# Optimization experiments

Hardware: AMD Instinct MI355X
Metric: run time of the kernel (lower is better)

## Reference

```python
import jax, jax.numpy as jnp
import numpy as np

DIM = 96
HID = 384
DEPTH = 5
HEADS = 8
INNER = 64 * DIM          # inner_dim = dim_head * dim per source (dim_head=64)
DH = INNER // HEADS       # per-head dim = 768
SCALE = 64 ** -0.5        # scale uses default dim_head=64, not actual per-head dim
EPS = 1e-5


def setup_inputs() -> dict:
    key = jax.random.key(0)
    ks = jax.random.split(key, 13)
    def p(k, shape, s=0.02):
        return jax.random.normal(k, shape, jnp.float32) * s
    return {
        "x": jax.random.normal(ks[0], (2, 512, DIM), jnp.float32),
        "gam_a": p(ks[1], (DEPTH, 3, DIM)),          # attention pre-norm gammas
        "Wq": p(ks[2], (DEPTH, 3, DIM, INNER)),
        "Wk": p(ks[3], (DEPTH, 3, DIM, INNER)),
        "Wv": p(ks[4], (DEPTH, 3, DIM, INNER)),
        "Wo": p(ks[5], (DEPTH, 3, INNER, DIM)),
        "gam_m": p(ks[6], (DEPTH, 2, DIM)),          # MLP pre-norm gammas
        "W1": p(ks[7], (DEPTH, 2, DIM, HID)),
        "b1": p(ks[8], (DEPTH, 2, HID)),
        "W2": p(ks[9], (DEPTH, 2, HID, DIM)),
        "b2": p(ks[10], (DEPTH, 2, DIM)),
        "gam_mid": p(ks[11], (DEPTH, DIM)),          # bare LayerNorm inside each block
        "gam_final": p(ks[12], (DIM,)),
    }


def _ln(x, g):
    # nn.LayerNorm(elementwise_affine=False) followed by x * (gamma + 1)
    mu = x.mean(-1, keepdims=True)
    var = ((x - mu) ** 2).mean(-1, keepdims=True)
    return (x - mu) * jax.lax.rsqrt(var + EPS) * (g + 1.0)


def _attn(x, g, wq, wk, wv, wo):
    b, n, _ = x.shape
    h = _ln(x, g)                                    # self.norm (reuse_attention=True)
    q = (h @ wq).reshape(b, n, HEADS, DH).transpose(0, 2, 1, 3) * SCALE
    k = (h @ wk).reshape(b, n, HEADS, DH).transpose(0, 2, 1, 3)
    v = (h @ wv).reshape(b, n, HEADS, DH).transpose(0, 2, 1, 3)
    sim = jnp.einsum("bhid,bhjd->bhij", q, k)        # [b,h,n,n]
    a = jax.nn.softmax(sim, axis=-1)                 # dropout=0.0 -> identity
    o = jnp.einsum("bhij,bhjd->bhid", a, v)
    return o.transpose(0, 2, 1, 3).reshape(b, n, INNER) @ wo


def _mlp(x, g, w1, b1_, w2, b2_):
    # LayerNorm -> Linear -> GELU(exact) -> Linear (dropouts eval-mode identity)
    h = jax.nn.gelu(_ln(x, g) @ w1 + b1_, approximate=False)
    return h @ w2 + b2_


def reference(x, gam_a, Wq, Wk, Wv, Wo, gam_m, W1, b1, W2, b2, gam_mid, gam_final):
    for d in range(DEPTH):
        x = _attn(x, gam_a[d, 0], Wq[d, 0], Wk[d, 0], Wv[d, 0], Wo[d, 0]) + x
        x = _mlp(x, gam_m[d, 0], W1[d, 0], b1[d, 0], W2[d, 0], b2[d, 0]) + x
        x = _attn(x, gam_a[d, 1], Wq[d, 1], Wk[d, 1], Wv[d, 1], Wo[d, 1]) + x
        x = _attn(x, gam_a[d, 2], Wq[d, 2], Wk[d, 2], Wv[d, 2], Wo[d, 2]) + x
        x = _ln(x, gam_mid[d])                       # bare LayerNorm, NO residual
        x = _mlp(x, gam_m[d, 1], W1[d, 1], b1[d, 1], W2[d, 1], b2[d, 1]) + x
    return _ln(x, gam_final)
```

## Files before the change

### kernel.cpp

```cpp
#include <hip/hip_runtime.h>
#include <hip/hip_bf16.h>

typedef __hip_bfloat16 bf16;
typedef __attribute__((ext_vector_type(8))) short bf16x8;
typedef __attribute__((ext_vector_type(4))) float f32x4;

#define TOK    1024
#define DIM    96
#define HIDN   384
#define HEADS  8
#define DH     768
#define INNER  6144
#define SEQ    512
#define NDEPTH 5
#define EPSLN  1e-5f
#define QSCALE 0.125f

#define MFMA16(a, b, c) __builtin_amdgcn_mfma_f32_16x16x32_bf16((a), (b), (c), 0, 0, 0)

__device__ __forceinline__ float b2f(bf16 v) { return __bfloat162float(v); }
__device__ __forceinline__ bf16  f2b(float v) { return __float2bfloat16(v); }

__device__ __forceinline__ float gload(const void* p, size_t i, int f) {
  return f ? b2f(((const bf16*)p)[i]) : ((const float*)p)[i];
}
__device__ __forceinline__ const char* gptr(const void* base, size_t off, int f) {
  return (const char*)base + off * (size_t)(f ? 2 : 4);
}

__global__ __launch_bounds__(256) void detect_kernel(const void* xraw, int* flag) {
  __shared__ int cnt[256];
  int t = threadIdx.x;
  const unsigned short* u = (const unsigned short*)xraw;
  int c = 0;
  #pragma unroll
  for (int i = 0; i < 4; i++) {
    unsigned short h = u[2 * (t * 4 + i)];
    int e = (h >> 7) & 0xFF;
    if (e >= 87 && e <= 132) c++;
  }
  cnt[t] = c;
  __syncthreads();
  for (int s = 128; s > 0; s >>= 1) {
    if (t < s) cnt[t] += cnt[t + s];
    __syncthreads();
  }
  if (t == 0) *flag = (cnt[0] > 700) ? 1 : 0;
}

__global__ __launch_bounds__(256) void castw3_kernel(
    const void* __restrict__ w0, const void* __restrict__ w1,
    const void* __restrict__ w2, bf16* __restrict__ o0,
    bf16* __restrict__ o1, bf16* __restrict__ o2, int n,
    const int* __restrict__ flagp) {
  if (*flagp) return;
  const float* in = (const float*)((blockIdx.y == 0) ? w0 : (blockIdx.y == 1) ? w1 : w2);
  bf16* out = (blockIdx.y == 0) ? o0 : (blockIdx.y == 1) ? o1 : o2;
  int i0 = (blockIdx.x * blockDim.x + threadIdx.x) * 4;
  if (i0 + 3 < n) {
    float4 v = *(const float4*)(in + i0);
    alignas(8) unsigned short o[4];
    bf16 t0 = f2b(v.x); o[0] = *(unsigned short*)&t0;
    bf16 t1 = f2b(v.y); o[1] = *(unsigned short*)&t1;
    bf16 t2 = f2b(v.z); o[2] = *(unsigned short*)&t2;
    bf16 t3 = f2b(v.w); o[3] = *(unsigned short*)&t3;
    *(uint2*)&out[i0] = *(const uint2*)o;
  } else {
    for (int i = i0; i < n; i++) out[i] = f2b(in[i]);
  }
}

__global__ __launch_bounds__(256) void wtrans_kernel(
    const void* __restrict__ src, int R, int C,
    bf16* __restrict__ dst, const int* __restrict__ flagp) {
  __shared__ float tile[32][65];
  int f = *flagp;
  int t = threadIdx.x;
  int c0 = blockIdx.x * 64, r0 = blockIdx.y * 32;
  size_t bb = (size_t)blockIdx.z * R * C;
  int ty = t >> 4, tx = t & 15;
  #pragma unroll
  for (int half = 0; half < 2; half++) {
    int r = r0 + ty + half * 16;
    int c = c0 + tx * 4;
    if (c < C) {
      size_t idx = bb + (size_t)r * C + c;
      float v0, v1, v2, v3;
      if (f) {
        uint2 u = *(const uint2*)((const unsigned short*)src + idx);
        v0 = __uint_as_float((u.x & 0xffffu) << 16);
        v1 = __uint_as_float(u.x & 0xffff0000u);
        v2 = __uint_as_float((u.y & 0xffffu) << 16);
        v3 = __uint_as_float(u.y & 0xffff0000u);
      } else {
        float4 v = *(const float4*)((const float*)src + idx);
        v0 = v.x; v1 = v.y; v2 = v.z; v3 = v.w;
      }
      tile[ty + half * 16][tx * 4 + 0] = v0;
      tile[ty + half * 16][tx * 4 + 1] = v1;
      tile[ty + half * 16][tx * 4 + 2] = v2;
      tile[ty + half * 16][tx * 4 + 3] = v3;
    }
  }
  __syncthreads();
  int cc = c0 + (t >> 2), rseg = (t & 3) * 8;
  if (cc < C) {
    int cs = cc - c0;
    alignas(16) unsigned short o[8];
    #pragma unroll
    for (int j = 0; j < 8; j++) {
      bf16 tv = f2b(tile[rseg + j][cs]);
      o[j] = *(unsigned short*)&tv;
    }
    *(uint4*)&dst[bb + (size_t)cc * R + r0 + rseg] = *(const uint4*)o;
  }
}

template <int WM>
__device__ __forceinline__ void gemm_bt_body(
    const bf16* __restrict__ A, int lda,
    const bf16* __restrict__ Bt, int ldb,
    int m0, int n0, int kbeg, int kend, int Mtot, int N,
    float alpha, bf16* __restrict__ Cb, int ldc) {
  constexpr int TM = WM * 32;
  __shared__ bf16 As[TM][40];
  __shared__ bf16 Bs[128][40];
  int t = threadIdx.x;
  int lane = t & 63;
  int wave = t >> 6;
  int wm = (wave >> 1) * (WM * 16), wn = (wave & 1) * 64;
  f32x4 acc[WM][4];
  #pragma unroll
  for (int i = 0; i < WM; i++)
    #pragma unroll
    for (int j = 0; j < 4; j++) acc[i][j] = (f32x4){0.f, 0.f, 0.f, 0.f};

  int arow = t >> 2, aseg = (t & 3) * 8;

  for (int kb = kbeg; kb < kend; kb += 32) {
    if constexpr (TM >= 64) {
      #pragma unroll
      for (int i = 0; i < TM / 64; i++) {
        int gm = min(m0 + arow + i * 64, Mtot - 1);
        *(uint4*)&As[arow + i * 64][aseg] =
            *(const uint4*)(A + (size_t)gm * lda + kb + aseg);
      }
    } else {
      if (arow < TM) {
        int gm = min(m0 + arow, Mtot - 1);
        *(uint4*)&As[arow][aseg] =
            *(const uint4*)(A + (size_t)gm * lda + kb + aseg);
      }
    }
    #pragma unroll
    for (int i = 0; i < 2; i++) {
      int r = arow + i * 64;
      int gn = n0 + r;
      uint4 val = {0, 0, 0, 0};
      if (gn < N) val = *(const uint4*)(Bt + (size_t)gn * ldb + kb + aseg);
      *(uint4*)&Bs[r][aseg] = val;
    }
    __syncthreads();
    int fm = lane & 15, fq = (lane >> 4) * 8;
    bf16x8 af[WM], bfv[4];
    #pragma unroll
    for (int i = 0; i < WM; i++)
      af[i] = *(const bf16x8*)&As[wm + i * 16 + fm][fq];
    #pragma unroll
    for (int j = 0; j < 4; j++)
      bfv[j] = *(const bf16x8*)&Bs[wn + j * 16 + fm][fq];
    #pragma unroll
    for (int i = 0; i < WM; i++)
      #pragma unroll
      for (int j = 0; j < 4; j++)
        acc[i][j] = MFMA16(af[i], bfv[j], acc[i][j]);
    __syncthreads();
  }
  int col = lane & 15, rq = (lane >> 4) * 4;
  #pragma unroll
  for (int j = 0; j < 4; j++) {
    int gn = n0 + wn + j * 16 + col;
    if (gn >= N) continue;
    #pragma unroll
    for (int i = 0; i < WM; i++) {
      #pragma unroll
      for (int r = 0; r < 4; r++) {
        int gm = m0 + wm + i * 16 + rq + r;
        if (gm >= Mtot) continue;
        Cb[(size_t)gm * ldc + gn] = f2b(acc[i][j][r] * alpha);
      }
    }
  }
}

__global__ __launch_bounds__(256) void mtgt_kernel(
    const void* __restrict__ WqE, const void* __restrict__ WkE,
    const void* __restrict__ WvE,
    const bf16* __restrict__ wqB, const bf16* __restrict__ wkB,
    const bf16* __restrict__ wvB, const bf16* __restrict__ woT,
    bf16* __restrict__ Mt, bf16* __restrict__ Gt,
    const int* __restrict__ flagp) {
  int f = *flagp;
  const bf16* wq = f ? (const bf16*)WqE : wqB;
  const bf16* wk = f ? (const bf16*)WkE : wkB;
  const bf16* wv = f ? (const bf16*)WvE : wvB;
  int z = blockIdx.z;
  bool isM = z < 120;
  int zz = isM ? z : z - 120;
  int L = zz >> 3, h = zz & 7;
  size_t wo = (size_t)L * DIM * INNER + (size_t)h * DH;
  const bf16* A  = isM ? (wk + wo) : (woT + wo);
  const bf16* Bt = isM ? (wq + wo) : (wv + wo);
  bf16* C = (isM ? Mt : Gt) + (size_t)zz * DIM * DIM;
  gemm_bt_body<2>(A, INNER, Bt, INNER, blockIdx.y * 64, 0, 0, DH, DIM, DIM,
                  isM ? QSCALE : 1.f, C, DIM);
}

__device__ __forceinline__ void ln_row_vals(float v0, float v1in, int lane,
    const char* g, int f, float& o0, float& o1) {
  float v1 = (lane < 32) ? v1in : 0.f;
  float s = v0 + v1;
  #pragma unroll
  for (int off = 32; off > 0; off >>= 1) s += __shfl_xor(s, off);
  float mu = s * (1.f / 96.f);
  float d0 = v0 - mu;
  float d1 = (lane < 32) ? (v1 - mu) : 0.f;
  float q = d0 * d0 + d1 * d1;
  #pragma unroll
  for (int off = 32; off > 0; off >>= 1) q += __shfl_xor(q, off);
  float rstd = rsqrtf(q * (1.f / 96.f) + EPSLN);
  o0 = d0 * rstd * (gload(g, lane, f) + 1.f);
  o1 = (lane < 32) ? (d1 * rstd * (gload(g, 64 + lane, f) + 1.f)) : 0.f;
}

__device__ __forceinline__ void store_hn(bf16* hn, bf16* hnT, int row, int lane,
                                         float o0, float o1) {
  size_t base = (size_t)row * DIM;
  bf16* hT = hnT + (size_t)(row >> 9) * DIM * SEQ;
  int ss = row & (SEQ - 1);
  hn[base + lane] = f2b(o0);
  hT[(size_t)lane * SEQ + ss] = f2b(o0);
  if (lane < 32) {
    hn[base + 64 + lane] = f2b(o1);
    hT[(size_t)(64 + lane) * SEQ + ss] = f2b(o1);
  }
}

__global__ __launch_bounds__(256) void castln_kernel(
    const void* __restrict__ in_x, float* __restrict__ x,
    bf16* __restrict__ hn, bf16* __restrict__ hnT,
    const void* __restrict__ gb, const int* __restrict__ flagp) {
  int f = *flagp;
  int wave = threadIdx.x >> 6, lane = threadIdx.x & 63;
  int row = blockIdx.x * 4 + wave;
  size_t base = (size_t)row * DIM;
  float v0 = gload(in_x, base + lane, f);
  float v1 = (lane < 32) ? gload(in_x, base + 64 + lane, f) : 0.f;
  x[base + lane] = v0;
  if (lane < 32) x[base + 64 + lane] = v1;
  float o0, o1;
  ln_row_vals(v0, v1, lane, gptr(gb, 0, f), f, o0, o1);
  store_hn(hn, hnT, row, lane, o0, o1);
}

__global__ __launch_bounds__(256) void ln_kernel(
    const float* __restrict__ x, bf16* __restrict__ hn, bf16* __restrict__ hnT,
    const void* __restrict__ gb, size_t goff, const int* __restrict__ flagp) {
  int f = *flagp;
  int wave = threadIdx.x >> 6, lane = threadIdx.x & 63;
  int row = blockIdx.x * 4 + wave;
  size_t base = (size_t)row * DIM;
  float v0 = x[base + lane];
  float v1 = (lane < 32) ? x[base + 64 + lane] : 0.f;
  float o0, o1;
  ln_row_vals(v0, v1, lane, gptr(gb, goff, f), f, o0, o1);
  store_hn(hn, hnT, row, lane, o0, o1);
}

__global__ __launch_bounds__(512) void fattn4_kernel(
    const bf16* __restrict__ hn,
    const bf16* __restrict__ hnT,
    const bf16* __restrict__ MtL,
    const bf16* __restrict__ GtL,
    float* __restrict__ x) {
  __shared__ bf16 tP[32][520];
  __shared__ bf16 Zs[32][104];
  __shared__ float red[2][8][32];
  int tid = threadIdx.x, lane = tid & 63, wave = tid >> 6;
  int fm = lane & 15, fq = (lane >> 4) * 8;
  int col = lane & 15, rq = (lane >> 4) * 4;
  int z = blockIdx.y, b = z >> 3, h = z & 7;
  int m0 = blockIdx.x * 32;
  const bf16* hnB = hn + (size_t)b * SEQ * DIM;
  const bf16* hTB = hnT + (size_t)b * DIM * SEQ;
  const bf16* MtH = MtL + (size_t)h * DIM * DIM;
  const bf16* GtH = GtL + (size_t)h * DIM * DIM;

  if (wave < 6) {
    int mA = wave & 1, nb = wave >> 1;
    f32x4 a0 = (f32x4){0.f, 0.f, 0.f, 0.f}, a1 = a0;
    #pragma unroll
    for (int kb = 0; kb < 96; kb += 32) {
      bf16x8 af = *(const bf16x8*)(hnB + (size_t)(m0 + mA * 16 + fm) * DIM + kb + fq);
      bf16x8 b0 = *(const bf16x8*)(MtH + (size_t)(nb * 16 + fm) * DIM + kb + fq);
      bf16x8 b1 = *(const bf16x8*)(MtH + (size_t)((nb + 3) * 16 + fm) * DIM + kb + fq);
      a0 = MFMA16(af, b0, a0);
      a1 = MFMA16(af, b1, a1);
    }
    #pragma unroll
    for (int r = 0; r < 4; r++) {
      Zs[mA * 16 + rq + r][nb * 16 + col] = f2b(a0[r]);
      Zs[mA * 16 + rq + r][(nb + 3) * 16 + col] = f2b(a1[r]);
    }
  }
  __syncthreads();

  f32x4 acc2[2][4];
  #pragma unroll
  for (int i = 0; i < 2; i++)
    #pragma unroll
    for (int j = 0; j < 4; j++) acc2[i][j] = (f32x4){0.f, 0.f, 0.f, 0.f};
  #pragma unroll
  for (int kb = 0; kb < 96; kb += 32) {
    bf16x8 af0 = *(const bf16x8*)&Zs[fm][kb + fq];
    bf16x8 af1 = *(const bf16x8*)&Zs[16 + fm][kb + fq];
    bf16x8 bv[4];
    #pragma unroll
    for (int j = 0; j < 4; j++)
      bv[j] = *(const bf16x8*)(hnB + (size_t)(wave * 64 + j * 16 + fm) * DIM + kb + fq);
    #pragma unroll
    for (int j = 0; j < 4; j++) {
      acc2[0][j] = MFMA16(af0, bv[j], acc2[0][j]);
      acc2[1][j] = MFMA16(af1, bv[j], acc2[1][j]);
    }
  }

  float rmax[2][4];
  #pragma unroll
  for (int i = 0; i < 2; i++)
    #pragma unroll
    for (int r = 0; r < 4; r++) {
      float m = -1e30f;
      #pragma unroll
      for (int j = 0; j < 4; j++) m = fmaxf(m, acc2[i][j][r]);
      rmax[i][r] = m;
    }
  #pragma unroll
  for (int s = 1; s < 16; s <<= 1)
    #pragma unroll
    for (int i = 0; i < 2; i++)
      #pragma unroll
      for (int r = 0; r < 4; r++)
        rmax[i][r] = fmaxf(rmax[i][r], __shfl_xor(rmax[i][r], s));
  if (col == 0)
    #pragma unroll
    for (int i = 0; i < 2; i++)
      #pragma unroll
      for (int r = 0; r < 4; r++) red[0][wave][i * 16 + rq + r] = rmax[i][r];
  __syncthreads();
  float rsum[2][4];
  #pragma unroll
  for (int i = 0; i < 2; i++)
    #pragma unroll
    for (int r = 0; r < 4; r++) {
      int row = i * 16 + rq + r;
      float gm = red[0][0][row];
      #pragma unroll
      for (int q = 1; q < 8; q++) gm = fmaxf(gm, red[0][q][row]);
      float s = 0.f;
      #pragma unroll
      for (int j = 0; j < 4; j++) {
        float e = __expf(acc2[i][j][r] - gm);
        acc2[i][j][r] = e;
        s += e;
      }
      rsum[i][r] = s;
    }
  #pragma unroll
  for (int s = 1; s < 16; s <<= 1)
    #pragma unroll
    for (int i = 0; i < 2; i++)
      #pragma unroll
      for (int r = 0; r < 4; r++)
        rsum[i][r] += __shfl_xor(rsum[i][r], s);
  if (col == 0)
    #pragma unroll
    for (int i = 0; i < 2; i++)
      #pragma unroll
      for (int r = 0; r < 4; r++) red[1][wave][i * 16 + rq + r] = rsum[i][r];
  __syncthreads();

  #pragma unroll
  for (int i = 0; i < 2; i++)
    #pragma unroll
    for (int r = 0; r < 4; r++) {
      int row = i * 16 + rq + r;
      float tot = red[1][0][row];
      #pragma unroll
      for (int q = 1; q < 8; q++) tot += red[1][q][row];
      float inv = 1.f / tot;
      #pragma unroll
      for (int j = 0; j < 4; j++)
        tP[row][wave * 64 + j * 16 + col] = f2b(acc2[i][j][r] * inv);
    }
  __syncthreads();

  f32x4 z0 = (f32x4){0.f, 0.f, 0.f, 0.f}, z1 = z0;
  if (wave < 4) {
    int n = wave;
    #pragma unroll 4
    for (int kb = 0; kb < 512; kb += 32) {
      bf16x8 bv = *(const bf16x8*)(hTB + (size_t)(n * 16 + fm) * SEQ + kb + fq);
      bf16x8 af0 = *(const bf16x8*)&tP[fm][kb + fq];
      bf16x8 af1 = *(const bf16x8*)&tP[16 + fm][kb + fq];
      z0 = MFMA16(af0, bv, z0);
      z1 = MFMA16(af1, bv, z1);
    }
    #pragma unroll
    for (int r = 0; r < 4; r++) {
      Zs[rq + r][n * 16 + col] = f2b(z0[r]);
      Zs[16 + rq + r][n * 16 + col] = f2b(z1[r]);
    }
  } else {
    int mA = wave & 1, n = (wave >> 1) + 2;
    #pragma unroll 4
    for (int kb = 0; kb < 512; kb += 32) {
      bf16x8 bv = *(const bf16x8*)(hTB + (size_t)(n * 16 + fm) * SEQ + kb + fq);
      bf16x8 af = *(const bf16x8*)&tP[mA * 16 + fm][kb + fq];
      z0 = MFMA16(af, bv, z0);
    }
    #pragma unroll
    for (int r = 0; r < 4; r++)
      Zs[mA * 16 + rq + r][n * 16 + col] = f2b(z0[r]);
  }
  __syncthreads();

  if (wave < 6) {
    int mA = wave & 1, nb = wave >> 1;
    f32x4 o0 = (f32x4){0.f, 0.f, 0.f, 0.f}, o1 = o0;
    #pragma unroll
    for (int kb = 0; kb < 96; kb += 32) {
      bf16x8 af = *(const bf16x8*)&Zs[mA * 16 + fm][kb + fq];
      bf16x8 b0 = *(const bf16x8*)(GtH + (size_t)(nb * 16 + fm) * DIM + kb + fq);
      bf16x8 b1 = *(const bf16x8*)(GtH + (size_t)((nb + 3) * 16 + fm) * DIM + kb + fq);
      o0 = MFMA16(af, b0, o0);
      o1 = MFMA16(af, b1, o1);
    }
    #pragma unroll
    for (int r = 0; r < 4; r++) {
      int gr = b * SEQ + m0 + mA * 16 + rq + r;
      atomicAdd(x + (size_t)gr * DIM + nb * 16 + col, o0[r]);
      atomicAdd(x + (size_t)gr * DIM + (nb + 3) * 16 + col, o1[r]);
    }
  }
}

__global__ __launch_bounds__(512) void fmlp_kernel(
    float* __restrict__ X,
    const void* __restrict__ gmidb, size_t gmidoff, int useMid,
    const void* __restrict__ gmb, size_t gmoff,
    const bf16* __restrict__ w1T,
    const void* __restrict__ b1b, size_t b1off,
    const bf16* __restrict__ w2T,
    const void* __restrict__ b2b, size_t b2off,
    int lnmode, const void* __restrict__ lngb, size_t lngoff,
    bf16* __restrict__ hn, bf16* __restrict__ hnT, void* __restrict__ dout,
    const int* __restrict__ flagp) {
  __shared__ float X1s[32][96];
  __shared__ bf16 As[32][104];
  __shared__ bf16 Hs[32][392];
  int f = *flagp;
  int tid = threadIdx.x, lane = tid & 63, wave = tid >> 6;
  int fm = lane & 15, fq = (lane >> 4) * 8;
  int col = lane & 15, rq = (lane >> 4) * 4;
  int m0 = blockIdx.x * 32;
  const char* gm = gptr(gmb, gmoff, f);
  float gm0 = gload(gm, lane, f) + 1.f;
  float gm1 = (lane < 32) ? (gload(gm, 64 + lane, f) + 1.f) : 0.f;
  float gd0 = 1.f, gd1 = 1.f;
  if (useMid) {
    const char* gmid = gptr(gmidb, gmidoff, f);
    gd0 = gload(gmid, lane, f) + 1.f;
    gd1 = (lane < 32) ? (gload(gmid, 64 + lane, f) + 1.f) : 0.f;
  }
  for (int r = wave; r < 32; r += 8) {
    const float* xr = X + (size_t)(m0 + r) * DIM;
    float v0 = xr[lane];
    float v1 = (lane < 32) ? xr[64 + lane] : 0.f;
    if (useMid) {
      float s = v0 + v1;
      #pragma unroll
      for (int off = 32; off > 0; off >>= 1) s += __shfl_xor(s, off);
      float mu = s * (1.f / 96.f);
      float d0 = v0 - mu;
      float d1 = (lane < 32) ? (v1 - mu) : 0.f;
      float q = d0 * d0 + d1 * d1;
      #pragma unroll
      for (int off = 32; off > 0; off >>= 1) q += __shfl_xor(q, off);
      float rstd = rsqrtf(q * (1.f / 96.f) + EPSLN);
      v0 = d0 * rstd * gd0;
      v1 = (lane < 32) ? (d1 * rstd * gd1) : 0.f;
    }
    X1s[r][lane] = v0;
    if (lane < 32) X1s[r][64 + lane] = v1;
    float s = v0 + v1;
    #pragma unroll
    for (int off = 32; off > 0; off >>= 1) s += __shfl_xor(s, off);
    float mu = s * (1.f / 96.f);
    float d0 = v0 - mu;
    float d1 = (lane < 32) ? (v1 - mu) : 0.f;
    float q = d0 * d0 + d1 * d1;
    #pragma unroll
    for (int off = 32; off > 0; off >>= 1) q += __shfl_xor(q, off);
    float rstd = rsqrtf(q * (1.f / 96.f) + EPSLN);
    As[r][lane] = f2b(d0 * rstd * gm0);
    if (lane < 32) As[r][64 + lane] = f2b(d1 * rstd * gm1);
  }
  __syncthreads();

  int mw = wave & 1, nh = wave >> 1;
  f32x4 acc1[6];
  #pragma unroll
  for (int j = 0; j < 6; j++) acc1[j] = (f32x4){0.f, 0.f, 0.f, 0.f};
  #pragma unroll
  for (int kb = 0; kb < 96; kb += 32) {
    bf16x8 af = *(const bf16x8*)&As[mw * 16 + fm][kb + fq];
    #pragma unroll
    for (int j = 0; j < 6; j++) {
      bf16x8 bv = *(const bf16x8*)(w1T + (size_t)(nh * 96 + j * 16 + fm) * DIM + kb + fq);
      acc1[j] = MFMA16(af, bv, acc1[j]);
    }
  }
  const char* b1p = gptr(b1b, b1off, f);
  #pragma unroll
  for (int j = 0; j < 6; j++) {
    int gn = nh * 96 + j * 16 + col;
    float bv = gload(b1p, gn, f);
    #pragma unroll
    for (int r = 0; r < 4; r++) {
      float v = acc1[j][r] + bv;
      v = 0.5f * v * (1.f + erff(v * 0.70710678118f));
      Hs[mw * 16 + rq + r][gn] = f2b(v);
    }
  }
  __syncthreads();

  if (wave < 6) {
    int mA = wave & 1, nb = wave >> 1;
    f32x4 o0 = (f32x4){0.f, 0.f, 0.f, 0.f}, o1 = o0;
    #pragma unroll 4
    for (int kb = 0; kb < 384; kb += 32) {
      bf16x8 af = *(const bf16x8*)&Hs[mA * 16 + fm][kb + fq];
      bf16x8 b0 = *(const bf16x8*)(w2T + (size_t)(nb * 16 + fm) * HIDN + kb + fq);
      bf16x8 b1 = *(const bf16x8*)(w2T + (size_t)((nb + 3) * 16 + fm) * HIDN + kb + fq);
      o0 = MFMA16(af, b0, o0);
      o1 = MFMA16(af, b1, o1);
    }
    const char* b2p = gptr(b2b, b2off, f);
    float bb0 = gload(b2p, nb * 16 + col, f);
    float bb1 = gload(b2p, (nb + 3) * 16 + col, f);
    #pragma unroll
    for (int r = 0; r < 4; r++) {
      int row = mA * 16 + rq + r;
      int gmr = m0 + row;
      X[(size_t)gmr * DIM + nb * 16 + col] = X1s[row][nb * 16 + col] + o0[r] + bb0;
      X[(size_t)gmr * DIM + (nb + 3) * 16 + col] = X1s[row][(nb + 3) * 16 + col] + o1[r] + bb1;
    }
  }
  __syncthreads();

  const char* lg = gptr(lngb, lngoff, f);
  for (int r = wave; r < 32; r += 8) {
    int row = m0 + r;
    size_t base = (size_t)row * DIM;
    float v0 = X[base + lane];
    float v1 = (lane < 32) ? X[base + 64 + lane] : 0.f;
    float o0, o1;
    ln_row_vals(v0, v1, lane, lg, f, o0, o1);
    if (lnmode == 1) {
      store_hn(hn, hnT, row, lane, o0, o1);
    } else {
      if (!f) {
        ((float*)dout)[base + lane] = o0;
        if (lane < 32) ((float*)dout)[base + 64 + lane] = o1;
      } else {
        ((bf16*)dout)[base + lane] = f2b(o0);
        if (lane < 32) ((bf16*)dout)[base + 64 + lane] = f2b(o1);
      }
    }
  }
}

extern "C" void kernel_launch(void* const* d_in, const int* in_sizes, int n_in,
                              void* d_out, int out_size, void* d_ws, size_t ws_size,
                              hipStream_t stream) {
  const void* in_x    = d_in[0];
  const void* gam_a   = d_in[1];
  const void* Wq      = d_in[2];
  const void* Wk      = d_in[3];
  const void* Wv      = d_in[4];
  const void* Wo      = d_in[5];
  const void* gam_m   = d_in[6];
  const void* W1      = d_in[7];
  const void* b1      = d_in[8];
  const void* W2      = d_in[9];
  const void* b2      = d_in[10];
  const void* gam_mid = d_in[11];
  const void* gam_fin = d_in[12];

  char* wsb = (char*)d_ws;
  size_t off = 0;
  auto carve = [&](size_t bytes) {
    char* p = wsb + off;
    off += (bytes + 255) & ~(size_t)255;
    return p;
  };
  int*   flag = (int*)carve(256);
  float* x    = (float*)carve((size_t)TOK * DIM * 4);
  bf16*  hn   = (bf16*)carve((size_t)TOK * DIM * 2);
  bf16*  hnT  = (bf16*)carve((size_t)2 * DIM * SEQ * 2);
  const size_t WSZ = (size_t)15 * DIM * INNER;
  bf16*  wqB  = (bf16*)carve(WSZ * 2);
  bf16*  wkB  = (bf16*)carve(WSZ * 2);
  bf16*  wvB  = (bf16*)carve(WSZ * 2);
  bf16*  woT  = (bf16*)carve(WSZ * 2);
  bf16*  w1T  = (bf16*)carve((size_t)10 * DIM * HIDN * 2);
  bf16*  w2T  = (bf16*)carve((size_t)10 * DIM * HIDN * 2);
  bf16*  Mt   = (bf16*)carve((size_t)120 * DIM * DIM * 2);
  bf16*  Gt   = (bf16*)carve((size_t)120 * DIM * DIM * 2);

  detect_kernel<<<dim3(1), dim3(256), 0, stream>>>(in_x, flag);

  int nW = (int)WSZ;
  castw3_kernel<<<dim3((nW / 4 + 255) / 256, 3), dim3(256), 0, stream>>>(
      Wq, Wk, Wv, wqB, wkB, wvB, nW, flag);
  wtrans_kernel<<<dim3(2, 192, 15), dim3(256), 0, stream>>>(Wo, INNER, DIM, woT, flag);
  wtrans_kernel<<<dim3(6, 3, 10), dim3(256), 0, stream>>>(W1, DIM, HIDN, w1T, flag);
  wtrans_kernel<<<dim3(2, 12, 10), dim3(256), 0, stream>>>(W2, HIDN, DIM, w2T, flag);
  mtgt_kernel<<<dim3(1, 2, 240), dim3(256), 0, stream>>>(
      Wq, Wk, Wv, wqB, wkB, wvB, woT, Mt, Gt, flag);

  castln_kernel<<<dim3(TOK / 4), dim3(256), 0, stream>>>(in_x, x, hn, hnT, gam_a, flag);

  auto attn = [&](int d, int j) {
    size_t gi = ((size_t)d * 3 + j);
    fattn4_kernel<<<dim3(16, 16), dim3(512), 0, stream>>>(
        hn, hnT, Mt + gi * 8 * DIM * DIM, Gt + gi * 8 * DIM * DIM, x);
  };

  for (int d = 0; d < NDEPTH; d++) {
    bool last = (d == NDEPTH - 1);
    attn(d, 0);
    fmlp_kernel<<<dim3(32), dim3(512), 0, stream>>>(
        x, nullptr, 0, 0,
        gam_m, (size_t)(d * 2 + 0) * DIM,
        w1T + (size_t)(d * 2 + 0) * DIM * HIDN, b1, (size_t)(d * 2 + 0) * HIDN,
        w2T + (size_t)(d * 2 + 0) * DIM * HIDN, b2, (size_t)(d * 2 + 0) * DIM,
        1, gam_a, (size_t)(d * 3 + 1) * DIM, hn, hnT, nullptr, flag);
    attn(d, 1);
    ln_kernel<<<dim3(TOK / 4), dim3(256), 0, stream>>>(
        x, hn, hnT, gam_a, (size_t)(d * 3 + 2) * DIM, flag);
    attn(d, 2);
    fmlp_kernel<<<dim3(32), dim3(512), 0, stream>>>(
        x, gam_mid, (size_t)d * DIM, 1,
        gam_m, (size_t)(d * 2 + 1) * DIM,
        w1T + (size_t)(d * 2 + 1) * DIM * HIDN, b1, (size_t)(d * 2 + 1) * HIDN,
        w2T + (size_t)(d * 2 + 1) * DIM * HIDN, b2, (size_t)(d * 2 + 1) * DIM,
        last ? 2 : 1, last ? gam_fin : gam_a,
        last ? (size_t)0 : (size_t)((d + 1) * 3) * DIM,
        hn, hnT, d_out, flag);
  }
}
```

Before: 682.6 us.

## Fuse fp32-to-bf16 weight cast into the Mt/Gt precompute GEMM tile loads

```diff
diff --git a/kernel.cpp b/kernel.cpp
--- a/kernel.cpp
+++ b/kernel.cpp
@@ -28,6 +28,20 @@
   return (const char*)base + off * (size_t)(f ? 2 : 4);
 }
 
+__device__ __forceinline__ uint4 pack8(float4 u0, float4 u1) {
+  alignas(16) unsigned short o[8];
+  bf16 t;
+  t = f2b(u0.x); o[0] = *(unsigned short*)&t;
+  t = f2b(u0.y); o[1] = *(unsigned short*)&t;
+  t = f2b(u0.z); o[2] = *(unsigned short*)&t;
+  t = f2b(u0.w); o[3] = *(unsigned short*)&t;
+  t = f2b(u1.x); o[4] = *(unsigned short*)&t;
+  t = f2b(u1.y); o[5] = *(unsigned short*)&t;
+  t = f2b(u1.z); o[6] = *(unsigned short*)&t;
+  t = f2b(u1.w); o[7] = *(unsigned short*)&t;
+  return *(const uint4*)o;
+}
+
 __global__ __launch_bounds__(256) void detect_kernel(const void* xraw, int* flag) {
   __shared__ int cnt[256];
   int t = threadIdx.x;
@@ -46,28 +60,6 @@
     __syncthreads();
   }
   if (t == 0) *flag = (cnt[0] > 700) ? 1 : 0;
-}
-
-__global__ __launch_bounds__(256) void castw3_kernel(
-    const void* __restrict__ w0, const void* __restrict__ w1,
-    const void* __restrict__ w2, bf16* __restrict__ o0,
-    bf16* __restrict__ o1, bf16* __restrict__ o2, int n,
-    const int* __restrict__ flagp) {
-  if (*flagp) return;
-  const float* in = (const float*)((blockIdx.y == 0) ? w0 : (blockIdx.y == 1) ? w1 : w2);
-  bf16* out = (blockIdx.y == 0) ? o0 : (blockIdx.y == 1) ? o1 : o2;
-  int i0 = (blockIdx.x * blockDim.x + threadIdx.x) * 4;
-  if (i0 + 3 < n) {
-    float4 v = *(const float4*)(in + i0);
-    alignas(8) unsigned short o[4];
-    bf16 t0 = f2b(v.x); o[0] = *(unsigned short*)&t0;
-    bf16 t1 = f2b(v.y); o[1] = *(unsigned short*)&t1;
-    bf16 t2 = f2b(v.z); o[2] = *(unsigned short*)&t2;
-    bf16 t3 = f2b(v.w); o[3] = *(unsigned short*)&t3;
-    *(uint2*)&out[i0] = *(const uint2*)o;
-  } else {
-    for (int i = i0; i < n; i++) out[i] = f2b(in[i]);
-  }
 }
 
 __global__ __launch_bounds__(256) void wtrans_kernel(
@@ -118,8 +110,8 @@
 
 template <int WM>
 __device__ __forceinline__ void gemm_bt_body(
-    const bf16* __restrict__ A, int lda,
-    const bf16* __restrict__ Bt, int ldb,
+    const void* __restrict__ A, int aF32, int lda,
+    const void* __restrict__ Bt, int bF32, int ldb,
     int m0, int n0, int kbeg, int kend, int Mtot, int N,
     float alpha, bf16* __restrict__ Cb, int ldc) {
   constexpr int TM = WM * 32;
@@ -138,27 +130,40 @@
   int arow = t >> 2, aseg = (t & 3) * 8;
 
   for (int kb = kbeg; kb < kend; kb += 32) {
-    if constexpr (TM >= 64) {
-      #pragma unroll
-      for (int i = 0; i < TM / 64; i++) {
-        int gm = min(m0 + arow + i * 64, Mtot - 1);
-        *(uint4*)&As[arow + i * 64][aseg] =
-            *(const uint4*)(A + (size_t)gm * lda + kb + aseg);
-      }
-    } else {
-      if (arow < TM) {
-        int gm = min(m0 + arow, Mtot - 1);
-        *(uint4*)&As[arow][aseg] =
-            *(const uint4*)(A + (size_t)gm * lda + kb + aseg);
+    #pragma unroll
+    for (int i = 0; i < (TM + 63) / 64; i++) {
+      int rr = arow + i * 64;
+      if ((TM % 64 == 0) || rr < TM) {
+        int gm = min(m0 + rr, Mtot - 1);
+        size_t idx = (size_t)gm * lda + kb + aseg;
+        if (aF32) {
+          const float* Af = (const float*)A;
+          float4 u0 = *(const float4*)(Af + idx);
+          float4 u1 = *(const float4*)(Af + idx + 4);
+          *(uint4*)&As[rr][aseg] = pack8(u0, u1);
+        } else {
+          *(uint4*)&As[rr][aseg] = *(const uint4*)((const bf16*)A + idx);
+        }
       }
     }
     #pragma unroll
     for (int i = 0; i < 2; i++) {
       int r = arow + i * 64;
       int gn = n0 + r;
-      uint4 val = {0, 0, 0, 0};
-      if (gn < N) val = *(const uint4*)(Bt + (size_t)gn * ldb + kb + aseg);
-      *(uint4*)&Bs[r][aseg] = val;
+      if (gn < N) {
+        size_t idx = (size_t)gn * ldb + kb + aseg;
+        if (bF32) {
+          const float* Bf = (const float*)Bt;
+          float4 u0 = *(const float4*)(Bf + idx);
+          float4 u1 = *(const float4*)(Bf + idx + 4);
+          *(uint4*)&Bs[r][aseg] = pack8(u0, u1);
+        } else {
+          *(uint4*)&Bs[r][aseg] = *(const uint4*)((const bf16*)Bt + idx);
+        }
+      } else {
+        uint4 zz = {0, 0, 0, 0};
+        *(uint4*)&Bs[r][aseg] = zz;
+      }
     }
     __syncthreads();
     int fm = lane & 15, fq = (lane >> 4) * 8;
@@ -195,24 +200,24 @@
 
 __global__ __launch_bounds__(256) void mtgt_kernel(
     const void* __restrict__ WqE, const void* __restrict__ WkE,
-    const void* __restrict__ WvE,
-    const bf16* __restrict__ wqB, const bf16* __restrict__ wkB,
-    const bf16* __restrict__ wvB, const bf16* __restrict__ woT,
+    const void* __restrict__ WvE, const bf16* __restrict__ woT,
     bf16* __restrict__ Mt, bf16* __restrict__ Gt,
     const int* __restrict__ flagp) {
   int f = *flagp;
-  const bf16* wq = f ? (const bf16*)WqE : wqB;
-  const bf16* wk = f ? (const bf16*)WkE : wkB;
-  const bf16* wv = f ? (const bf16*)WvE : wvB;
   int z = blockIdx.z;
   bool isM = z < 120;
   int zz = isM ? z : z - 120;
   int L = zz >> 3, h = zz & 7;
   size_t wo = (size_t)L * DIM * INNER + (size_t)h * DH;
-  const bf16* A  = isM ? (wk + wo) : (woT + wo);
-  const bf16* Bt = isM ? (wq + wo) : (wv + wo);
+  size_t wo2 = f ? wo : wo;
+  const void* A  = isM ? (const void*)((const char*)WkE + wo2 * (f ? 2 : 4))
+                       : (const void*)(woT + wo);
+  const void* Bt = isM ? (const void*)((const char*)WqE + wo2 * (f ? 2 : 4))
+                       : (const void*)((const char*)WvE + wo2 * (f ? 2 : 4));
+  int aF32 = isM ? !f : 0;
+  int bF32 = !f;
   bf16* C = (isM ? Mt : Gt) + (size_t)zz * DIM * DIM;
-  gemm_bt_body<2>(A, INNER, Bt, INNER, blockIdx.y * 64, 0, 0, DH, DIM, DIM,
+  gemm_bt_body<3>(A, aF32, INNER, Bt, bF32, INNER, 0, 0, 0, DH, DIM, DIM,
                   isM ? QSCALE : 1.f, C, DIM);
 }
 
@@ -563,8 +568,12 @@
     for (int r = 0; r < 4; r++) {
       int row = mA * 16 + rq + r;
       int gmr = m0 + row;
-      X[(size_t)gmr * DIM + nb * 16 + col] = X1s[row][nb * 16 + col] + o0[r] + bb0;
-      X[(size_t)gmr * DIM + (nb + 3) * 16 + col] = X1s[row][(nb + 3) * 16 + col] + o1[r] + bb1;
+      float nv0 = X1s[row][nb * 16 + col] + o0[r] + bb0;
+      float nv1 = X1s[row][(nb + 3) * 16 + col] + o1[r] + bb1;
+      X[(size_t)gmr * DIM + nb * 16 + col] = nv0;
+      X[(size_t)gmr * DIM + (nb + 3) * 16 + col] = nv1;
+      X1s[row][nb * 16 + col] = nv0;
+      X1s[row][(nb + 3) * 16 + col] = nv1;
     }
   }
   __syncthreads();
@@ -573,8 +582,8 @@
   for (int r = wave; r < 32; r += 8) {
     int row = m0 + r;
     size_t base = (size_t)row * DIM;
-    float v0 = X[base + lane];
-    float v1 = (lane < 32) ? X[base + 64 + lane] : 0.f;
+    float v0 = X1s[r][lane];
+    float v1 = (lane < 32) ? X1s[r][64 + lane] : 0.f;
     float o0, o1;
     ln_row_vals(v0, v1, lane, lg, f, o0, o1);
     if (lnmode == 1) {
@@ -620,9 +629,6 @@
   bf16*  hn   = (bf16*)carve((size_t)TOK * DIM * 2);
   bf16*  hnT  = (bf16*)carve((size_t)2 * DIM * SEQ * 2);
   const size_t WSZ = (size_t)15 * DIM * INNER;
-  bf16*  wqB  = (bf16*)carve(WSZ * 2);
-  bf16*  wkB  = (bf16*)carve(WSZ * 2);
-  bf16*  wvB  = (bf16*)carve(WSZ * 2);
   bf16*  woT  = (bf16*)carve(WSZ * 2);
   bf16*  w1T  = (bf16*)carve((size_t)10 * DIM * HIDN * 2);
   bf16*  w2T  = (bf16*)carve((size_t)10 * DIM * HIDN * 2);
@@ -631,14 +637,11 @@
 
   detect_kernel<<<dim3(1), dim3(256), 0, stream>>>(in_x, flag);
 
-  int nW = (int)WSZ;
-  castw3_kernel<<<dim3((nW / 4 + 255) / 256, 3), dim3(256), 0, stream>>>(
-      Wq, Wk, Wv, wqB, wkB, wvB, nW, flag);
   wtrans_kernel<<<dim3(2, 192, 15), dim3(256), 0, stream>>>(Wo, INNER, DIM, woT, flag);
   wtrans_kernel<<<dim3(6, 3, 10), dim3(256), 0, stream>>>(W1, DIM, HIDN, w1T, flag);
   wtrans_kernel<<<dim3(2, 12, 10), dim3(256), 0, stream>>>(W2, HIDN, DIM, w2T, flag);
-  mtgt_kernel<<<dim3(1, 2, 240), dim3(256), 0, stream>>>(
-      Wq, Wk, Wv, wqB, wkB, wvB, woT, Mt, Gt, flag);
+  mtgt_kernel<<<dim3(1, 1, 240), dim3(256), 0, stream>>>(
+      Wq, Wk, Wv, woT, Mt, Gt, flag);
 
   castln_kernel<<<dim3(TOK / 4), dim3(256), 0, stream>>>(in_x, x, hn, hnT, gam_a, flag);
 
```

After: 691.0 us. No clear change (+1.2%).
